# Optimization experiments

Measured on AMD Instinct MI355X. Metric: run time of the kernel, lower is better.

Reference implementation:

```python
import jax, jax.numpy as jnp
import numpy as np

EPS = 2e-05
N_H_RDG = 9   # lifting scale grid: h_j = 2**j, j=0..8
N_H_CROP = 3  # group-conv scale support: offsets 0,1,2 (dyadic index shifts)


def _scaled_kernel(w, h):
    """Resample base kernel w [O, I, K] (taps on integers centered at 0) at
    coordinates x/h via linear interpolation -> [O, I, (K-1)*h+1], with the
    R+ Haar-measure normalization 1/h (psi_h(x) = psi(x/h)/h)."""
    K = w.shape[-1]
    Kh = (K - 1) * h + 1
    m = jnp.arange(K, dtype=jnp.float32) - K // 2
    x = (jnp.arange(Kh, dtype=jnp.float32) - Kh // 2) / h
    hat = jnp.maximum(0.0, 1.0 - jnp.abs(x[:, None] - m[None, :]))  # [Kh, K]
    return jnp.einsum('oim,xm->oix', w, hat) / h


def _conv1d_same(x, k):
    pad = (k.shape[-1] - 1) // 2
    return jax.lax.conv_general_dilated(
        x, k, window_strides=(1,), padding=[(pad, pad)],
        dimension_numbers=('NCH', 'OIH', 'NCH'))


def _pool_r1(x, stride):
    # max pool over the spatial (last) axis only: kernel 4, pad 1 each side
    return jax.lax.reduce_window(
        x, -jnp.inf, jax.lax.max,
        window_dimensions=(1, 1, 1, 4), window_strides=(1, 1, 1, stride),
        padding=((0, 0), (0, 0), (0, 0), (1, 1)))


def _bn(x, g, b):
    # BatchNorm2d over [B, C, H_scale, L], training-mode batch stats
    mu = jnp.mean(x, axis=(0, 2, 3), keepdims=True)
    var = jnp.var(x, axis=(0, 2, 3), keepdims=True)
    return (x - mu) * jax.lax.rsqrt(var + EPS) * g[None, :, None, None] + b[None, :, None, None]


def _forward(x, w1, w2, w3, g1, b1, g2, b2, g3, b3, fw1, fb1, fw2, fb2, fw3, fb3):
    B = x.shape[0]
    # --- c1: GConvRdG lifting, scales h_j = 2**j, j=0..8 ---
    out = jnp.stack([_conv1d_same(x, _scaled_kernel(w1, 2 ** j))
                     for j in range(N_H_RDG)], axis=2)      # [B,16,9,16]
    out = _bn(jax.nn.relu(_pool_r1(out, 2)), g1, b1)        # [B,16,9,8]
    # --- c2: GConvGG, h_crop=True: out scale j uses in scales j..j+2 ---
    O2, I2 = w2.shape[0], w2.shape[1]
    w2r = w2.reshape(O2, I2 * N_H_CROP, 3)
    H2 = out.shape[2] - (N_H_CROP - 1)  # 7
    out = jnp.stack([
        _conv1d_same(out[:, :, j:j + N_H_CROP, :].reshape(B, I2 * N_H_CROP, -1),
                     _scaled_kernel(w2r, 2 ** j))
        for j in range(H2)], axis=2)                        # [B,32,7,8]
    out = _bn(jax.nn.relu(_pool_r1(out, 2)), g2, b2)        # [B,32,7,4]
    # --- c3: GConvGG with 1x1 spatial kernel ---
    w3s = w3[:, :, :, 0]  # [64,32,3]
    H3 = out.shape[2] - (N_H_CROP - 1)  # 5
    out = jnp.stack([
        jnp.einsum('oik,bikl->bol', w3s, out[:, :, j:j + N_H_CROP, :]) / (2.0 ** j)
        for j in range(H3)], axis=2)                        # [B,64,5,4]
    out = _bn(jax.nn.relu(_pool_r1(out, 4)), g3, b3)        # [B,64,5,1]
    # --- MLP head (dropout is identity in eval) ---
    out = out.reshape(B, -1)                                # [B,320]
    out = out @ fw1.T + fb1
    out = out @ fw2.T + fb2
    return out @ fw3.T + fb3                                # [B,17]


def setup_inputs() -> dict:
    key = jax.random.key(0)
    ks = jax.random.split(key, 7)
    B = 4096
    x = jax.random.normal(ks[0], (B, 6, 16), dtype=jnp.float32)
    w1 = jax.random.normal(ks[1], (16, 6, 7), dtype=jnp.float32) * (6 * 7) ** -0.5
    w2 = jax.random.normal(ks[2], (32, 16, 3, 3), dtype=jnp.float32) * (16 * 3 * 3) ** -0.5
    w3 = jax.random.normal(ks[3], (64, 32, 3, 1), dtype=jnp.float32) * (32 * 3) ** -0.5
    fw1 = jax.random.normal(ks[4], (16, 320), dtype=jnp.float32) * 320 ** -0.5
    fw2 = jax.random.normal(ks[5], (16, 16), dtype=jnp.float32) * 16 ** -0.5
    fw3 = jax.random.normal(ks[6], (17, 16), dtype=jnp.float32) * 16 ** -0.5
    return {
        'x': x, 'w1': w1, 'w2': w2, 'w3': w3,
        'g1': jnp.ones(16), 'b1': jnp.zeros(16),
        'g2': jnp.ones(32), 'b2': jnp.zeros(32),
        'g3': jnp.ones(64), 'b3': jnp.zeros(64),
        'fw1': fw1, 'fb1': jnp.zeros(16),
        'fw2': fw2, 'fb2': jnp.zeros(16),
        'fw3': fw3, 'fb3': jnp.zeros(17),
    }


def reference(x, w1, w2, w3, g1, b1, g2, b2, g3, b3, fw1, fb1, fw2, fb2, fw3, fb3):
    return _forward(x, w1, w2, w3, g1, b1, g2, b2, g3, b3, fw1, fb1, fw2, fb2, fw3, fb3)
```

## Files before the change

kernel.cpp:

```cpp
#include <hip/hip_runtime.h>

#define EPS 2e-5f

using short8  = __attribute__((ext_vector_type(8))) short;
using floatx4 = __attribute__((ext_vector_type(4))) float;

static __device__ inline unsigned short f2bf(float f) {
    unsigned u = __float_as_uint(f);
    u += 0x7fffu + ((u >> 16) & 1u);
    return (unsigned short)(u >> 16);
}
static __device__ inline float bf2f(short s) {
    return __uint_as_float(((unsigned)(unsigned short)s) << 16);
}
static __device__ inline short8 scale8(short8 v, float sc) {
    short8 r;
    #pragma unroll
    for (int e = 0; e < 8; ++e) r[e] = (short)f2bf(bf2f(v[e]) * sc);
    return r;
}


__global__ void __launch_bounds__(256) kSa(const float* __restrict__ w1,
                                           unsigned short* __restrict__ W1f,
                                           float* __restrict__ stats) {
    int gid = blockIdx.x * 256 + threadIdx.x;
    if (gid < 256) stats[gid] = 0.f;
    int j  = gid / 24576;
    int r  = gid % 24576;
    int T  = r / 1536;
    int r2 = r % 1536;
    int ks = r2 / 512;
    int r3 = r2 % 512;
    int ln = r3 >> 3, e = r3 & 7;
    int n  = T * 16 + (ln & 15);
    int kk = ks * 32 + (ln >> 4) * 8 + e;
    int o = n >> 4, t = n & 15;
    int i = kk >> 4, s = kk & 15;
    int h = 1 << j;
    int d = s - t;
    float val = 0.f;
    if (d >= -3 * h && d <= 3 * h) {
        float df = (float)d / (float)h;
        #pragma unroll
        for (int m = 0; m < 7; ++m) {
            float hat = fmaxf(0.f, 1.f - fabsf(df - (float)(m - 3)));
            val += w1[(o * 6 + i) * 7 + m] * hat;
        }
        val /= (float)h;
    }
    W1f[gid] = f2bf(val);
}

__global__ void __launch_bounds__(256) k1(const float* __restrict__ x,
                                          const unsigned short* __restrict__ W1f,
                                          const float* __restrict__ w2,
                                          unsigned short* __restrict__ p1,
                                          unsigned short* __restrict__ W2r,
                                          float* __restrict__ S,
                                          float* __restrict__ stats1, int B) {
    __shared__ float z[32 * 276];
    __shared__ float lsS[256], lsQ[256];
    int tid = threadIdx.x;

    if (blockIdx.y == 9) {
        int base = blockIdx.x * 256 + tid;
        for (int g = base; g < 688128; g += 32768) {
            int fs = g >> 9;
            int ln = (g >> 3) & 63, e = g & 7;
            int j  = fs / 192;
            int rm = fs % 192;
            int T  = rm / 12, ks = rm % 12;
            int col = T * 16 + (ln & 15);
            int k   = ks * 32 + (ln >> 4) * 8 + e;
            int o = col >> 3, t = col & 7;
            int ic = k >> 3, s = k & 7;
            int i = ic / 3, c = ic % 3;
            int h = 1 << j;
            int d = s - t;
            float raw = 0.f;
            if (d >= -h && d <= h) {
                float df = (float)d / (float)h;
                #pragma unroll
                for (int m = 0; m < 3; ++m) {
                    float hat = fmaxf(0.f, 1.f - fabsf(df - (float)(m - 1)));
                    raw += w2[((o * 16 + i) * 3 + c) * 3 + m] * hat;
                }
                raw /= (float)h;
            }
            W2r[g] = f2bf(raw);
        }
        for (int g = base; g < 28672; g += 32768) {
            int j = g >> 12;
            int r = g & 4095;
            int i = r >> 8;
            int col = r & 255;
            int o = col >> 3, t = col & 7;
            int h = 1 << j;
            float acc = 0.f;
            #pragma unroll
            for (int c = 0; c < 3; ++c) {
                const float* wr = &w2[((o * 16 + i) * 3 + c) * 3];
                #pragma unroll
                for (int s = 0; s < 8; ++s) {
                    int d = s - t;
                    if (d >= -h && d <= h) {
                        float df = (float)d / (float)h;
                        float raw = 0.f;
                        #pragma unroll
                        for (int m = 0; m < 3; ++m) {
                            float hat = fmaxf(0.f, 1.f - fabsf(df - (float)(m - 1)));
                            raw += wr[m] * hat;
                        }
                        acc += raw / (float)h;
                    }
                }
            }
            S[g] = acc;
        }
        return;
    }

    int j = blockIdx.y;
    int wav = tid >> 6, lane = tid & 63;
    int quad = lane >> 4, l15 = lane & 15;
    int msub = wav & 1, nh = wav >> 1;
    int b0 = blockIdx.x * 32;
    floatx4 acc[8];
    #pragma unroll
    for (int T = 0; T < 8; ++T) acc[T] = floatx4{0.f, 0.f, 0.f, 0.f};
    const float* xr = x + (size_t)(b0 + msub * 16 + l15) * 96;
    const short8* Bj = (const short8*)W1f + (size_t)(j * 16) * 3 * 64;
    #pragma unroll
    for (int ks = 0; ks < 3; ++ks) {
        int k0 = ks * 32 + quad * 8;
        floatx4 v0 = *(const floatx4*)(xr + k0);
        floatx4 v1 = *(const floatx4*)(xr + k0 + 4);
        short8 a;
        #pragma unroll
        for (int e = 0; e < 4; ++e) {
            a[e]     = (short)f2bf(v0[e]);
            a[e + 4] = (short)f2bf(v1[e]);
        }
        #pragma unroll
        for (int T = 0; T < 8; ++T) {
            short8 b = Bj[((nh * 8 + T) * 3 + ks) * 64 + lane];
            acc[T] = __builtin_amdgcn_mfma_f32_16x16x32_bf16(a, b, acc[T], 0, 0, 0);
        }
    }
    #pragma unroll
    for (int T = 0; T < 8; ++T) {
        int col = (nh * 8 + T) * 16 + l15;
        int rb  = msub * 16 + quad * 4;
        #pragma unroll
        for (int r = 0; r < 4; ++r) z[(rb + r) * 276 + col] = acc[T][r];
    }
    __syncthreads();
    float psum = 0.f, pss = 0.f;
    #pragma unroll
    for (int i = 0; i < 2; ++i) {
        int u = tid + 256 * i;
        int row = u >> 4, o = u & 15;
        const float* zr = &z[row * 276 + o * 16];
        floatx4 q0 = ((const floatx4*)zr)[0];
        floatx4 q1 = ((const floatx4*)zr)[1];
        floatx4 q2 = ((const floatx4*)zr)[2];
        floatx4 q3 = ((const floatx4*)zr)[3];
        float t[16] = {q0[0], q0[1], q0[2], q0[3], q1[0], q1[1], q1[2], q1[3],
                       q2[0], q2[1], q2[2], q2[3], q3[0], q3[1], q3[2], q3[3]};
        short8 pk;
        #pragma unroll
        for (int tp = 0; tp < 8; ++tp) {
            int lo = (tp == 0) ? 0 : 2 * tp - 1;
            int hi = (tp == 7) ? 15 : 2 * tp + 2;
            float m = t[lo];
            for (int tt = lo + 1; tt <= hi; ++tt) m = fmaxf(m, t[tt]);
            m = fmaxf(m, 0.f);
            pk[tp] = (short)f2bf(m);
            psum += m; pss += m * m;
        }
        *(short8*)(p1 + ((size_t)j * B + b0 + row) * 128 + o * 8) = pk;
    }
    lsS[(tid & 15) * 16 + (tid >> 4)] = psum;
    lsQ[(tid & 15) * 16 + (tid >> 4)] = pss;
    __syncthreads();
    if (tid < 32) {
        int o = tid & 15;
        const float* src = (tid < 16) ? lsS : lsQ;
        float s = 0.f;
        #pragma unroll
        for (int g = 0; g < 16; ++g) s += src[o * 16 + g];
        atomicAdd(&stats1[(tid < 16 ? 0 : 16) + o], s);
    }
}

__global__ void __launch_bounds__(256) k2(const unsigned short* __restrict__ p1,
                                          const unsigned short* __restrict__ W2r,
                                          const float* __restrict__ S,
                                          const float* __restrict__ g1,
                                          const float* __restrict__ b1,
                                          const float* __restrict__ stats1,
                                          unsigned short* __restrict__ p2s,
                                          float* __restrict__ stats2,
                                          float invN1, int B) {
    __shared__ float z[32 * 260];
    __shared__ float lsS[512], lsQ[512];
    __shared__ float a1s[16], d1s[16], bias2L[256];
    int tid = threadIdx.x, j = blockIdx.y;
    int wav = tid >> 6, lane = tid & 63;
    int quad = lane >> 4, l15 = lane & 15;
    int nh = wav & 1, mp = wav >> 1;
    int b0 = blockIdx.x * 64, m0 = b0 + mp * 32;
    if (tid < 16) {
        float mu  = stats1[tid] * invN1;
        float var = stats1[16 + tid] * invN1 - mu * mu;
        float rs  = rsqrtf(var + EPS);
        a1s[tid] = g1[tid] * rs;
        d1s[tid] = b1[tid] - mu * a1s[tid];
    }
    __syncthreads();
    {
        float s = 0.f;
        const float* Sj = S + (size_t)j * 4096;
        #pragma unroll
        for (int i = 0; i < 16; ++i) s = fmaf(d1s[i], Sj[i * 256 + tid], s);
        bias2L[tid] = s;
    }
    __syncthreads();
    float biasv[8];
    #pragma unroll
    for (int T = 0; T < 8; ++T) biasv[T] = bias2L[(nh * 8 + T) * 16 + l15];
    floatx4 acc[2][8];
    #pragma unroll
    for (int mi = 0; mi < 2; ++mi)
        #pragma unroll
        for (int T = 0; T < 8; ++T) acc[mi][T] = floatx4{0.f, 0.f, 0.f, 0.f};
    const short8* Bj = (const short8*)W2r + (size_t)(j * 16) * 12 * 64;
    #pragma unroll
    for (int ks = 0; ks < 12; ++ks) {
        int icq = ks * 4 + quad;
        int i = icq / 3, c = icq - i * 3;
        float a1v = a1s[i];
        const unsigned short* ap = p1 + ((size_t)(j + c) * B + m0 + l15) * 128 + i * 8;
        short8 a0 = scale8(*(const short8*)ap, a1v);
        short8 a1 = scale8(*(const short8*)(ap + 2048), a1v);
        #pragma unroll
        for (int T = 0; T < 8; ++T) {
            short8 b = Bj[((nh * 8 + T) * 12 + ks) * 64 + lane];
            acc[0][T] = __builtin_amdgcn_mfma_f32_16x16x32_bf16(a0, b, acc[0][T], 0, 0, 0);
            acc[1][T] = __builtin_amdgcn_mfma_f32_16x16x32_bf16(a1, b, acc[1][T], 0, 0, 0);
        }
    }
    float psum[2] = {0.f, 0.f}, pss[2] = {0.f, 0.f};
    for (int pass = 0; pass < 2; ++pass) {
        __syncthreads();
        if (mp == pass) {
            #pragma unroll
            for (int T = 0; T < 8; ++T) {
                int col = (nh * 8 + T) * 16 + l15;
                #pragma unroll
                for (int mi = 0; mi < 2; ++mi) {
                    int rb = mi * 16 + quad * 4;
                    #pragma unroll
                    for (int r = 0; r < 4; ++r)
                        z[(rb + r) * 260 + col] = acc[mi][T][r] + biasv[T];
                }
            }
        }
        __syncthreads();
        #pragma unroll
        for (int i2 = 0; i2 < 2; ++i2) {
            int u = tid + 256 * i2;
            int opr = u & 15, row = u >> 4;
            const float* zr = &z[row * 260 + opr * 16];
            floatx4 q0 = ((const floatx4*)zr)[0];
            floatx4 q1 = ((const floatx4*)zr)[1];
            floatx4 q2 = ((const floatx4*)zr)[2];
            floatx4 q3 = ((const floatx4*)zr)[3];
            float ta[8] = {q0[0], q0[1], q0[2], q0[3], q1[0], q1[1], q1[2], q1[3]};
            float tb[8] = {q2[0], q2[1], q2[2], q2[3], q3[0], q3[1], q3[2], q3[3]};
            int rowg = pass * 32 + row;
            #pragma unroll
            for (int tp = 0; tp < 4; ++tp) {
                int lo = (tp == 0) ? 0 : 2 * tp - 1;
                int hi = (tp == 3) ? 7 : 2 * tp + 2;
                float m0v = ta[lo], m1v = tb[lo];
                for (int tt = lo + 1; tt <= hi; ++tt) {
                    m0v = fmaxf(m0v, ta[tt]); m1v = fmaxf(m1v, tb[tt]);
                }
                m0v = fmaxf(m0v, 0.f); m1v = fmaxf(m1v, 0.f);
                psum[0] += m0v; pss[0] += m0v * m0v;
                psum[1] += m1v; pss[1] += m1v * m1v;
                unsigned pk = (unsigned)f2bf(m0v) | ((unsigned)f2bf(m1v) << 16);
                *(unsigned*)(p2s + ((size_t)(j * 4 + tp) * B + b0 + rowg) * 32
                             + opr * 2) = pk;
            }
        }
    }
    {
        int o0 = 2 * (tid & 15), g = tid >> 4;
        lsS[o0 * 16 + g] = psum[0]; lsS[(o0 + 1) * 16 + g] = psum[1];
        lsQ[o0 * 16 + g] = pss[0];  lsQ[(o0 + 1) * 16 + g] = pss[1];
    }
    __syncthreads();
    if (tid < 64) {
        int o = tid & 31;
        const float* src = (tid < 32) ? lsS : lsQ;
        float s = 0.f;
        #pragma unroll
        for (int g = 0; g < 16; ++g) s += src[o * 16 + g];
        atomicAdd(&stats2[(tid < 32 ? 0 : 32) + o], s);
    }
}

__global__ void __launch_bounds__(256) k3(const unsigned short* __restrict__ p2s,
                                          const float* __restrict__ w3,
                                          const float* __restrict__ g2,
                                          const float* __restrict__ b2,
                                          const float* __restrict__ stats2,
                                          unsigned short* __restrict__ act3,
                                          float* __restrict__ stats3,
                                          float invN2, int B) {
    __shared__ float w3s[6144];
    __shared__ float a2s[32], d2s[32];
    __shared__ unsigned short atile[32][72];
    __shared__ float lsS[1024], lsQ[1024];
    int tid = threadIdx.x, j = blockIdx.y, b0 = blockIdx.x * 32;
    int og = tid >> 6, lane = tid & 63;
    int quad = lane >> 4, l15 = lane & 15;
    #pragma unroll
    for (int u = 0; u < 6; ++u) {
        int idx = tid * 4 + u * 1024;
        *(floatx4*)&w3s[idx] = *(const floatx4*)&w3[idx];
    }
    if (tid < 32) {
        float mu  = stats2[tid] * invN2;
        float var = stats2[32 + tid] * invN2 - mu * mu;
        float rs  = rsqrtf(var + EPS);
        a2s[tid] = g2[tid] * rs;
        d2s[tid] = b2[tid] - mu * a2s[tid];
    }
    __syncthreads();
    int o = og * 16 + l15;
    float biasacc = 0.f;
    short8 af[3];
    #pragma unroll
    for (int kf = 0; kf < 3; ++kf) {
        short8 v;
        #pragma unroll
        for (int e = 0; e < 8; ++e) {
            int i = quad * 8 + e;
            float raw = w3s[o * 96 + i * 3 + kf];
            v[e] = (short)f2bf(raw * a2s[i]);
            biasacc = fmaf(raw, d2s[i], biasacc);
        }
        af[kf] = v;
    }
    biasacc += __shfl_xor(biasacc, 16, 64);
    biasacc += __shfl_xor(biasacc, 32, 64);
    float brow[4];
    #pragma unroll
    for (int r = 0; r < 4; ++r) brow[r] = __shfl(biasacc, quad * 4 + r, 64);
    float inv = 1.f / (float)(1 << j);
    float psum[4] = {0.f, 0.f, 0.f, 0.f}, pss[4] = {0.f, 0.f, 0.f, 0.f};
    #pragma unroll
    for (int bt = 0; bt < 2; ++bt) {
        int bb = b0 + bt * 16;
        floatx4 aL0 = {0.f, 0.f, 0.f, 0.f};
        floatx4 aL1 = {0.f, 0.f, 0.f, 0.f};
        floatx4 aL2 = {0.f, 0.f, 0.f, 0.f};
        #pragma unroll
        for (int c = 0; c < 3; ++c) {
            const unsigned short* base =
                p2s + ((size_t)((j + c) * 4) * B + bb + l15) * 32 + quad * 8;
            short8 f0 = *(const short8*)base;
            short8 f1 = *(const short8*)(base + (size_t)B * 32);
            short8 f2v = *(const short8*)(base + (size_t)2 * B * 32);
            aL0 = __builtin_amdgcn_mfma_f32_16x16x32_bf16(af[c], f0, aL0, 0, 0, 0);
            aL1 = __builtin_amdgcn_mfma_f32_16x16x32_bf16(af[c], f1, aL1, 0, 0, 0);
            aL2 = __builtin_amdgcn_mfma_f32_16x16x32_bf16(af[c], f2v, aL2, 0, 0, 0);
        }
        #pragma unroll
        for (int r = 0; r < 4; ++r) {
            float vm = fmaxf(fmaxf(aL0[r], aL1[r]), aL2[r]);
            float v  = fmaxf((vm + brow[r]) * inv, 0.f);
            atile[bt * 16 + l15][og * 16 + quad * 4 + r] = f2bf(v);
            psum[r] += v; pss[r] += v * v;
        }
    }
    #pragma unroll
    for (int r = 0; r < 4; ++r) {
        lsS[(og * 16 + quad * 4 + r) * 16 + l15] = psum[r];
        lsQ[(og * 16 + quad * 4 + r) * 16 + l15] = pss[r];
    }
    __syncthreads();
    {
        int row = tid >> 3, oct = tid & 7;
        *(short8*)(act3 + ((size_t)j * B + b0 + row) * 64 + oct * 8) =
            *(const short8*)&atile[row][oct * 8];
    }
    if (tid < 128) {
        int oo = tid & 63;
        const float* src = (tid < 64) ? lsS : lsQ;
        float s = 0.f;
        #pragma unroll
        for (int g = 0; g < 16; ++g) s += src[oo * 16 + g];
        atomicAdd(&stats3[(tid < 64 ? 0 : 64) + oo], s);
    }
}

__global__ void __launch_bounds__(128) k4(const unsigned short* __restrict__ act3,
                                          const float* __restrict__ g3,
                                          const float* __restrict__ b3,
                                          const float* __restrict__ stats3,
                                          const float* __restrict__ fw1,
                                          const float* __restrict__ fb1,
                                          const float* __restrict__ fw2,
                                          const float* __restrict__ fb2,
                                          const float* __restrict__ fw3,
                                          const float* __restrict__ fb3,
                                          float* __restrict__ out,
                                          float invN3, int B) {
    __shared__ float fw1L[5120];
    __shared__ float a3s[64], d3s[64];
    __shared__ unsigned short W1s[5120];
    __shared__ float fw2s[256], fw3s[272], fb2s[16], fb3s[17], fb1f[16], tmp[4][16];
    __shared__ float hbuf[2][16][17];
    int tid = threadIdx.x;
    int wav = tid >> 6, lane = tid & 63;
    int quad = lane >> 4, l15 = lane & 15;
    #pragma unroll
    for (int u = 0; u < 10; ++u) {
        int idx = (tid + u * 128) * 4;
        *(floatx4*)&fw1L[idx] = *(const floatx4*)&fw1[idx];
    }
    if (tid < 64) {
        float mu  = stats3[tid] * invN3;
        float var = stats3[64 + tid] * invN3 - mu * mu;
        float rs  = rsqrtf(var + EPS);
        a3s[tid] = g3[tid] * rs;
        d3s[tid] = b3[tid] - mu * a3s[tid];
    }
    if (tid < 16) fb2s[tid] = fb2[tid];
    if (tid < 17) fb3s[tid] = fb3[tid];
    #pragma unroll
    for (int u = 0; u < 2; ++u) fw2s[tid + u * 128] = fw2[tid + u * 128];
    for (int idx = tid; idx < 272; idx += 128) fw3s[idx] = fw3[idx];
    __syncthreads();
    #pragma unroll
    for (int u = 0; u < 40; ++u) {
        int idx = tid + u * 128;
        int e  = idx & 7;
        int ln = (idx >> 3) & 63;
        int fs = idx >> 9;
        int jj = fs >> 1, ks = fs & 1;
        int n = ln & 15;
        int oo = ks * 32 + (ln >> 4) * 8 + e;
        W1s[idx] = f2bf(fw1L[n * 320 + oo * 5 + jj] * a3s[oo]);
    }
    if (tid < 64) {
        int f = tid & 15, ch = tid >> 4;
        float s = 0.f;
        for (int u = 0; u < 80; ++u) {
            int n = ch * 80 + u;
            s = fmaf(fw1L[f * 320 + n], d3s[n / 5], s);
        }
        tmp[ch][f] = s;
    }
    __syncthreads();
    if (tid < 16) fb1f[tid] = fb1[tid] + tmp[0][tid] + tmp[1][tid] + tmp[2][tid] + tmp[3][tid];
    __syncthreads();
    int mt = blockIdx.x * 2 + wav;
    floatx4 acc = {0.f, 0.f, 0.f, 0.f};
    #pragma unroll
    for (int jj = 0; jj < 5; ++jj)
        #pragma unroll
        for (int ks = 0; ks < 2; ++ks) {
            short8 a = *(const short8*)(act3 +
                ((size_t)jj * B + mt * 16 + l15) * 64 + ks * 32 + quad * 8);
            short8 b = *(const short8*)&W1s[((jj * 2 + ks) * 64 + lane) * 8];
            acc = __builtin_amdgcn_mfma_f32_16x16x32_bf16(a, b, acc, 0, 0, 0);
        }
    #pragma unroll
    for (int r = 0; r < 4; ++r) hbuf[wav][quad * 4 + r][l15] = acc[r] + fb1f[l15];
    __syncthreads();
    if (lane < 16) {
        int row = l15;
        float hv[16];
        #pragma unroll
        for (int n = 0; n < 16; ++n) hv[n] = hbuf[wav][row][n];
        float h2[16];
        #pragma unroll
        for (int f2 = 0; f2 < 16; ++f2) {
            float s = fb2s[f2];
            #pragma unroll
            for (int n = 0; n < 16; ++n) s = fmaf(fw2s[f2 * 16 + n], hv[n], s);
            h2[f2] = s;
        }
        float* orow = out + (size_t)(mt * 16 + row) * 17;
        #pragma unroll
        for (int f3 = 0; f3 < 17; ++f3) {
            float s = fb3s[f3];
            #pragma unroll
            for (int n = 0; n < 16; ++n) s = fmaf(fw3s[f3 * 16 + n], h2[n], s);
            orow[f3] = s;
        }
    }
}

extern "C" void kernel_launch(void* const* d_in, const int* in_sizes, int n_in,
                              void* d_out, int out_size, void* d_ws, size_t ws_size,
                              hipStream_t stream) {
    (void)n_in; (void)out_size; (void)ws_size;
    const float* x   = (const float*)d_in[0];
    const float* w1  = (const float*)d_in[1];
    const float* w2  = (const float*)d_in[2];
    const float* w3  = (const float*)d_in[3];
    const float* g1  = (const float*)d_in[4];
    const float* b1  = (const float*)d_in[5];
    const float* g2  = (const float*)d_in[6];
    const float* b2  = (const float*)d_in[7];
    const float* g3  = (const float*)d_in[8];
    const float* b3  = (const float*)d_in[9];
    const float* fw1 = (const float*)d_in[10];
    const float* fb1 = (const float*)d_in[11];
    const float* fw2 = (const float*)d_in[12];
    const float* fb2 = (const float*)d_in[13];
    const float* fw3 = (const float*)d_in[14];
    const float* fb3 = (const float*)d_in[15];
    float* out = (float*)d_out;

    int B = in_sizes[0] / 96;

    char* wsb = (char*)d_ws;
    float*          stats = (float*)wsb;
    unsigned short* W1f   = (unsigned short*)(wsb + 1024);
    unsigned short* W2r   = W1f + 221184;
    float*          S     = (float*)(W2r + 688128);
    unsigned short* p1    = (unsigned short*)(S + 28672);
    unsigned short* p2s   = p1 + (size_t)9 * B * 128;
    unsigned short* act3  = p2s + (size_t)28 * B * 32;

    float* stats1 = stats;
    float* stats2 = stats + 32;
    float* stats3 = stats + 96;

    float invN1 = 1.f / (float)(B * 72);
    float invN2 = 1.f / (float)(B * 28);
    float invN3 = 1.f / (float)(B * 5);

    kSa<<<864, 256, 0, stream>>>(w1, W1f, stats);
    k1<<<dim3(B / 32, 10), 256, 0, stream>>>(x, W1f, w2, p1, W2r, S, stats1, B);
    k2<<<dim3(B / 64, 7), 256, 0, stream>>>(p1, W2r, S, g1, b1, stats1, p2s, stats2,
                                            invN1, B);
    k3<<<dim3(B / 32, 5), 256, 0, stream>>>(p2s, w3, g2, b2, stats2, act3, stats3,
                                            invN2, B);
    k4<<<B / 32, 128, 0, stream>>>(act3, g3, b3, stats3, fw1, fb1, fw2, fb2, fw3, fb3,
                                   out, invN3, B);
}
```

Measured before the change: 174.4 us.

## Pre-permute w3/fw1 into MFMA fragment order and shrink k2/k3/k4 per-block work

```diff
diff --git a/kernel.cpp b/kernel.cpp
--- a/kernel.cpp
+++ b/kernel.cpp
@@ -55,9 +55,13 @@
 __global__ void __launch_bounds__(256) k1(const float* __restrict__ x,
                                           const unsigned short* __restrict__ W1f,
                                           const float* __restrict__ w2,
+                                          const float* __restrict__ w3,
+                                          const float* __restrict__ fw1,
                                           unsigned short* __restrict__ p1,
                                           unsigned short* __restrict__ W2r,
                                           float* __restrict__ S,
+                                          float* __restrict__ W3fF,
+                                          float* __restrict__ W1rF,
                                           float* __restrict__ stats1, int B) {
     __shared__ float z[32 * 276];
     __shared__ float lsS[256], lsQ[256];
@@ -118,6 +122,20 @@
             }
             S[g] = acc;
         }
+        for (int g = base; g < 6144; g += 32768) {
+            int e = g & 7, ln = (g >> 3) & 63, fo = g >> 9;
+            int kf = fo >> 2, og = fo & 3;
+            int o = og * 16 + (ln & 15);
+            int i = (ln >> 4) * 8 + e;
+            W3fF[g] = w3[(o * 32 + i) * 3 + kf];
+        }
+        for (int g = base; g < 5120; g += 32768) {
+            int e = g & 7, ln = (g >> 3) & 63, fo = g >> 9;
+            int jj = fo >> 1, ks = fo & 1;
+            int n = ln & 15;
+            int oo = ks * 32 + (ln >> 4) * 8 + e;
+            W1rF[g] = fw1[n * 320 + oo * 5 + jj];
+        }
         return;
     }
 
@@ -203,10 +221,11 @@
                                           unsigned short* __restrict__ p2s,
                                           float* __restrict__ stats2,
                                           float invN1, int B) {
-    __shared__ float z[32 * 260];
+    __shared__ float z[32 * 132];
     __shared__ float lsS[512], lsQ[512];
     __shared__ float a1s[16], d1s[16], bias2L[256];
-    int tid = threadIdx.x, j = blockIdx.y;
+    int tid = threadIdx.x;
+    int j = blockIdx.y >> 1, ch = blockIdx.y & 1;
     int wav = tid >> 6, lane = tid & 63;
     int quad = lane >> 4, l15 = lane & 15;
     int nh = wav & 1, mp = wav >> 1;
@@ -227,14 +246,15 @@
         bias2L[tid] = s;
     }
     __syncthreads();
-    float biasv[8];
-    #pragma unroll
-    for (int T = 0; T < 8; ++T) biasv[T] = bias2L[(nh * 8 + T) * 16 + l15];
-    floatx4 acc[2][8];
+    float biasv[4];
+    #pragma unroll
+    for (int T = 0; T < 4; ++T)
+        biasv[T] = bias2L[(ch * 8 + nh * 4 + T) * 16 + l15];
+    floatx4 acc[2][4];
     #pragma unroll
     for (int mi = 0; mi < 2; ++mi)
         #pragma unroll
-        for (int T = 0; T < 8; ++T) acc[mi][T] = floatx4{0.f, 0.f, 0.f, 0.f};
+        for (int T = 0; T < 4; ++T) acc[mi][T] = floatx4{0.f, 0.f, 0.f, 0.f};
     const short8* Bj = (const short8*)W2r + (size_t)(j * 16) * 12 * 64;
     #pragma unroll
     for (int ks = 0; ks < 12; ++ks) {
@@ -245,8 +265,8 @@
         short8 a0 = scale8(*(const short8*)ap, a1v);
         short8 a1 = scale8(*(const short8*)(ap + 2048), a1v);
         #pragma unroll
-        for (int T = 0; T < 8; ++T) {
-            short8 b = Bj[((nh * 8 + T) * 12 + ks) * 64 + lane];
+        for (int T = 0; T < 4; ++T) {
+            short8 b = Bj[((ch * 8 + nh * 4 + T) * 12 + ks) * 64 + lane];
             acc[0][T] = __builtin_amdgcn_mfma_f32_16x16x32_bf16(a0, b, acc[0][T], 0, 0, 0);
             acc[1][T] = __builtin_amdgcn_mfma_f32_16x16x32_bf16(a1, b, acc[1][T], 0, 0, 0);
         }
@@ -256,23 +276,21 @@
         __syncthreads();
         if (mp == pass) {
             #pragma unroll
-            for (int T = 0; T < 8; ++T) {
-                int col = (nh * 8 + T) * 16 + l15;
+            for (int T = 0; T < 4; ++T) {
+                int colloc = (nh * 4 + T) * 16 + l15;
                 #pragma unroll
                 for (int mi = 0; mi < 2; ++mi) {
                     int rb = mi * 16 + quad * 4;
                     #pragma unroll
                     for (int r = 0; r < 4; ++r)
-                        z[(rb + r) * 260 + col] = acc[mi][T][r] + biasv[T];
+                        z[(rb + r) * 132 + colloc] = acc[mi][T][r] + biasv[T];
                 }
             }
         }
         __syncthreads();
-        #pragma unroll
-        for (int i2 = 0; i2 < 2; ++i2) {
-            int u = tid + 256 * i2;
-            int opr = u & 15, row = u >> 4;
-            const float* zr = &z[row * 260 + opr * 16];
+        {
+            int opr = tid & 7, row = tid >> 3;
+            const float* zr = &z[row * 132 + opr * 16];
             floatx4 q0 = ((const floatx4*)zr)[0];
             floatx4 q1 = ((const floatx4*)zr)[1];
             floatx4 q2 = ((const floatx4*)zr)[2];
@@ -293,66 +311,75 @@
                 psum[1] += m1v; pss[1] += m1v * m1v;
                 unsigned pk = (unsigned)f2bf(m0v) | ((unsigned)f2bf(m1v) << 16);
                 *(unsigned*)(p2s + ((size_t)(j * 4 + tp) * B + b0 + rowg) * 32
-                             + opr * 2) = pk;
+                             + ch * 16 + opr * 2) = pk;
             }
         }
     }
     {
-        int o0 = 2 * (tid & 15), g = tid >> 4;
-        lsS[o0 * 16 + g] = psum[0]; lsS[(o0 + 1) * 16 + g] = psum[1];
-        lsQ[o0 * 16 + g] = pss[0];  lsQ[(o0 + 1) * 16 + g] = pss[1];
-    }
-    __syncthreads();
-    if (tid < 64) {
-        int o = tid & 31;
-        const float* src = (tid < 32) ? lsS : lsQ;
+        int opr = tid & 7, row = tid >> 3;
+        lsS[(opr * 2 + 0) * 32 + row] = psum[0];
+        lsS[(opr * 2 + 1) * 32 + row] = psum[1];
+        lsQ[(opr * 2 + 0) * 32 + row] = pss[0];
+        lsQ[(opr * 2 + 1) * 32 + row] = pss[1];
+    }
+    __syncthreads();
+    if (tid < 32) {
+        int oloc = tid & 15;
+        const float* src = (tid < 16) ? lsS : lsQ;
         float s = 0.f;
         #pragma unroll
-        for (int g = 0; g < 16; ++g) s += src[o * 16 + g];
-        atomicAdd(&stats2[(tid < 32 ? 0 : 32) + o], s);
+        for (int r = 0; r < 32; ++r) s += src[oloc * 32 + r];
+        atomicAdd(&stats2[(tid < 16 ? 0 : 32) + ch * 16 + oloc], s);
     }
 }
 
 __global__ void __launch_bounds__(256) k3(const unsigned short* __restrict__ p2s,
-                                          const float* __restrict__ w3,
+                                          const float* __restrict__ W3fF,
                                           const float* __restrict__ g2,
                                           const float* __restrict__ b2,
                                           const float* __restrict__ stats2,
                                           unsigned short* __restrict__ act3,
                                           float* __restrict__ stats3,
                                           float invN2, int B) {
-    __shared__ float w3s[6144];
-    __shared__ float a2s[32], d2s[32];
-    __shared__ unsigned short atile[32][72];
+    __shared__ unsigned short atile[16][72];
     __shared__ float lsS[1024], lsQ[1024];
-    int tid = threadIdx.x, j = blockIdx.y, b0 = blockIdx.x * 32;
+    int tid = threadIdx.x, j = blockIdx.y, b0 = blockIdx.x * 16;
     int og = tid >> 6, lane = tid & 63;
     int quad = lane >> 4, l15 = lane & 15;
-    #pragma unroll
-    for (int u = 0; u < 6; ++u) {
-        int idx = tid * 4 + u * 1024;
-        *(floatx4*)&w3s[idx] = *(const floatx4*)&w3[idx];
-    }
-    if (tid < 32) {
-        float mu  = stats2[tid] * invN2;
-        float var = stats2[32 + tid] * invN2 - mu * mu;
-        float rs  = rsqrtf(var + EPS);
-        a2s[tid] = g2[tid] * rs;
-        d2s[tid] = b2[tid] - mu * a2s[tid];
-    }
-    __syncthreads();
-    int o = og * 16 + l15;
+    int i0 = quad * 8;
+    floatx4 sm0 = *(const floatx4*)&stats2[i0];
+    floatx4 sm1 = *(const floatx4*)&stats2[i0 + 4];
+    floatx4 sq0 = *(const floatx4*)&stats2[32 + i0];
+    floatx4 sq1 = *(const floatx4*)&stats2[32 + i0 + 4];
+    floatx4 gg0 = *(const floatx4*)&g2[i0];
+    floatx4 gg1 = *(const floatx4*)&g2[i0 + 4];
+    floatx4 bv0 = *(const floatx4*)&b2[i0];
+    floatx4 bv1 = *(const floatx4*)&b2[i0 + 4];
+    float a2v[8], d2v[8];
+    #pragma unroll
+    for (int e = 0; e < 4; ++e) {
+        float mu = sm0[e] * invN2;
+        float var = sq0[e] * invN2 - mu * mu;
+        float rs = rsqrtf(var + EPS);
+        a2v[e] = gg0[e] * rs; d2v[e] = bv0[e] - mu * a2v[e];
+        mu = sm1[e] * invN2;
+        var = sq1[e] * invN2 - mu * mu;
+        rs = rsqrtf(var + EPS);
+        a2v[e + 4] = gg1[e] * rs; d2v[e + 4] = bv1[e] - mu * a2v[e + 4];
+    }
     float biasacc = 0.f;
     short8 af[3];
     #pragma unroll
     for (int kf = 0; kf < 3; ++kf) {
+        const float* wp = &W3fF[((size_t)(kf * 4 + og) * 64 + lane) * 8];
+        floatx4 w0 = ((const floatx4*)wp)[0];
+        floatx4 w1 = ((const floatx4*)wp)[1];
+        float wr[8] = {w0[0], w0[1], w0[2], w0[3], w1[0], w1[1], w1[2], w1[3]};
         short8 v;
         #pragma unroll
         for (int e = 0; e < 8; ++e) {
-            int i = quad * 8 + e;
-            float raw = w3s[o * 96 + i * 3 + kf];
-            v[e] = (short)f2bf(raw * a2s[i]);
-            biasacc = fmaf(raw, d2s[i], biasacc);
+            v[e] = (short)f2bf(wr[e] * a2v[e]);
+            biasacc = fmaf(wr[e], d2v[e], biasacc);
         }
         af[kf] = v;
     }
@@ -363,30 +390,26 @@
     for (int r = 0; r < 4; ++r) brow[r] = __shfl(biasacc, quad * 4 + r, 64);
     float inv = 1.f / (float)(1 << j);
     float psum[4] = {0.f, 0.f, 0.f, 0.f}, pss[4] = {0.f, 0.f, 0.f, 0.f};
-    #pragma unroll
-    for (int bt = 0; bt < 2; ++bt) {
-        int bb = b0 + bt * 16;
-        floatx4 aL0 = {0.f, 0.f, 0.f, 0.f};
-        floatx4 aL1 = {0.f, 0.f, 0.f, 0.f};
-        floatx4 aL2 = {0.f, 0.f, 0.f, 0.f};
-        #pragma unroll
-        for (int c = 0; c < 3; ++c) {
-            const unsigned short* base =
-                p2s + ((size_t)((j + c) * 4) * B + bb + l15) * 32 + quad * 8;
-            short8 f0 = *(const short8*)base;
-            short8 f1 = *(const short8*)(base + (size_t)B * 32);
-            short8 f2v = *(const short8*)(base + (size_t)2 * B * 32);
-            aL0 = __builtin_amdgcn_mfma_f32_16x16x32_bf16(af[c], f0, aL0, 0, 0, 0);
-            aL1 = __builtin_amdgcn_mfma_f32_16x16x32_bf16(af[c], f1, aL1, 0, 0, 0);
-            aL2 = __builtin_amdgcn_mfma_f32_16x16x32_bf16(af[c], f2v, aL2, 0, 0, 0);
-        }
-        #pragma unroll
-        for (int r = 0; r < 4; ++r) {
-            float vm = fmaxf(fmaxf(aL0[r], aL1[r]), aL2[r]);
-            float v  = fmaxf((vm + brow[r]) * inv, 0.f);
-            atile[bt * 16 + l15][og * 16 + quad * 4 + r] = f2bf(v);
-            psum[r] += v; pss[r] += v * v;
-        }
+    floatx4 aL0 = {0.f, 0.f, 0.f, 0.f};
+    floatx4 aL1 = {0.f, 0.f, 0.f, 0.f};
+    floatx4 aL2 = {0.f, 0.f, 0.f, 0.f};
+    #pragma unroll
+    for (int c = 0; c < 3; ++c) {
+        const unsigned short* base =
+            p2s + ((size_t)((j + c) * 4) * B + b0 + l15) * 32 + quad * 8;
+        short8 f0 = *(const short8*)base;
+        short8 f1 = *(const short8*)(base + (size_t)B * 32);
+        short8 f2v = *(const short8*)(base + (size_t)2 * B * 32);
+        aL0 = __builtin_amdgcn_mfma_f32_16x16x32_bf16(af[c], f0, aL0, 0, 0, 0);
+        aL1 = __builtin_amdgcn_mfma_f32_16x16x32_bf16(af[c], f1, aL1, 0, 0, 0);
+        aL2 = __builtin_amdgcn_mfma_f32_16x16x32_bf16(af[c], f2v, aL2, 0, 0, 0);
+    }
+    #pragma unroll
+    for (int r = 0; r < 4; ++r) {
+        float vm = fmaxf(fmaxf(aL0[r], aL1[r]), aL2[r]);
+        float v  = fmaxf((vm + brow[r]) * inv, 0.f);
+        atile[l15][og * 16 + quad * 4 + r] = f2bf(v);
+        psum[r] += v; pss[r] += v * v;
     }
     #pragma unroll
     for (int r = 0; r < 4; ++r) {
@@ -394,7 +417,7 @@
         lsQ[(og * 16 + quad * 4 + r) * 16 + l15] = pss[r];
     }
     __syncthreads();
-    {
+    if (tid < 128) {
         int row = tid >> 3, oct = tid & 7;
         *(short8*)(act3 + ((size_t)j * B + b0 + row) * 64 + oct * 8) =
             *(const short8*)&atile[row][oct * 8];
@@ -409,68 +432,53 @@
     }
 }
 
-__global__ void __launch_bounds__(128) k4(const unsigned short* __restrict__ act3,
-                                          const float* __restrict__ g3,
-                                          const float* __restrict__ b3,
-                                          const float* __restrict__ stats3,
-                                          const float* __restrict__ fw1,
-                                          const float* __restrict__ fb1,
-                                          const float* __restrict__ fw2,
-                                          const float* __restrict__ fb2,
-                                          const float* __restrict__ fw3,
-                                          const float* __restrict__ fb3,
-                                          float* __restrict__ out,
-                                          float invN3, int B) {
-    __shared__ float fw1L[5120];
-    __shared__ float a3s[64], d3s[64];
-    __shared__ unsigned short W1s[5120];
-    __shared__ float fw2s[256], fw3s[272], fb2s[16], fb3s[17], fb1f[16], tmp[4][16];
-    __shared__ float hbuf[2][16][17];
+__global__ void __launch_bounds__(64) k4(const unsigned short* __restrict__ act3,
+                                         const float* __restrict__ W1rF,
+                                         const float* __restrict__ g3,
+                                         const float* __restrict__ b3,
+                                         const float* __restrict__ stats3,
+                                         const float* __restrict__ fw1,
+                                         const float* __restrict__ fb1,
+                                         const float* __restrict__ fw2,
+                                         const float* __restrict__ fb2,
+                                         const float* __restrict__ fw3,
+                                         const float* __restrict__ fb3,
+                                         float* __restrict__ out,
+                                         float invN3, int B) {
+    __shared__ float a3s[64], d3s[64], fb1f[16], tmp[4][16];
+    __shared__ float fw2s[256], fw3s[272], fb2s[16], fb3s[17];
+    __shared__ float hbuf[16][17];
     int tid = threadIdx.x;
-    int wav = tid >> 6, lane = tid & 63;
-    int quad = lane >> 4, l15 = lane & 15;
-    #pragma unroll
-    for (int u = 0; u < 10; ++u) {
-        int idx = (tid + u * 128) * 4;
-        *(floatx4*)&fw1L[idx] = *(const floatx4*)&fw1[idx];
-    }
-    if (tid < 64) {
+    int quad = tid >> 4, l15 = tid & 15;
+    {
         float mu  = stats3[tid] * invN3;
         float var = stats3[64 + tid] * invN3 - mu * mu;
         float rs  = rsqrtf(var + EPS);
-        a3s[tid] = g3[tid] * rs;
-        d3s[tid] = b3[tid] - mu * a3s[tid];
-    }
+        float a   = g3[tid] * rs;
+        a3s[tid] = a;
+        d3s[tid] = b3[tid] - mu * a;
+    }
+    #pragma unroll
+    for (int u = 0; u < 4; ++u) fw2s[tid + u * 64] = fw2[tid + u * 64];
+    for (int idx = tid; idx < 272; idx += 64) fw3s[idx] = fw3[idx];
     if (tid < 16) fb2s[tid] = fb2[tid];
     if (tid < 17) fb3s[tid] = fb3[tid];
-    #pragma unroll
-    for (int u = 0; u < 2; ++u) fw2s[tid + u * 128] = fw2[tid + u * 128];
-    for (int idx = tid; idx < 272; idx += 128) fw3s[idx] = fw3[idx];
-    __syncthreads();
-    #pragma unroll
-    for (int u = 0; u < 40; ++u) {
-        int idx = tid + u * 128;
-        int e  = idx & 7;
-        int ln = (idx >> 3) & 63;
-        int fs = idx >> 9;
-        int jj = fs >> 1, ks = fs & 1;
-        int n = ln & 15;
-        int oo = ks * 32 + (ln >> 4) * 8 + e;
-        W1s[idx] = f2bf(fw1L[n * 320 + oo * 5 + jj] * a3s[oo]);
-    }
-    if (tid < 64) {
+    __syncthreads();
+    {
         int f = tid & 15, ch = tid >> 4;
         float s = 0.f;
         for (int u = 0; u < 80; ++u) {
             int n = ch * 80 + u;
-            s = fmaf(fw1L[f * 320 + n], d3s[n / 5], s);
+            s = fmaf(fw1[f * 320 + n], d3s[n / 5], s);
         }
         tmp[ch][f] = s;
     }
-    __syncthreads();
-    if (tid < 16) fb1f[tid] = fb1[tid] + tmp[0][tid] + tmp[1][tid] + tmp[2][tid] + tmp[3][tid];
-    __syncthreads();
-    int mt = blockIdx.x * 2 + wav;
+    float a3v[2][8];
+    #pragma unroll
+    for (int ks = 0; ks < 2; ++ks)
+        #pragma unroll
+        for (int e = 0; e < 8; ++e) a3v[ks][e] = a3s[ks * 32 + quad * 8 + e];
+    int mt = blockIdx.x;
     floatx4 acc = {0.f, 0.f, 0.f, 0.f};
     #pragma unroll
     for (int jj = 0; jj < 5; ++jj)
@@ -478,17 +486,29 @@
         for (int ks = 0; ks < 2; ++ks) {
             short8 a = *(const short8*)(act3 +
                 ((size_t)jj * B + mt * 16 + l15) * 64 + ks * 32 + quad * 8);
-            short8 b = *(const short8*)&W1s[((jj * 2 + ks) * 64 + lane) * 8];
+            const float* wp = &W1rF[((size_t)(jj * 2 + ks) * 64 + tid) * 8];
+            floatx4 w0 = ((const floatx4*)wp)[0];
+            floatx4 w1 = ((const floatx4*)wp)[1];
+            short8 b;
+            #pragma unroll
+            for (int e = 0; e < 4; ++e) {
+                b[e]     = (short)f2bf(w0[e] * a3v[ks][e]);
+                b[e + 4] = (short)f2bf(w1[e] * a3v[ks][e + 4]);
+            }
             acc = __builtin_amdgcn_mfma_f32_16x16x32_bf16(a, b, acc, 0, 0, 0);
         }
-    #pragma unroll
-    for (int r = 0; r < 4; ++r) hbuf[wav][quad * 4 + r][l15] = acc[r] + fb1f[l15];
-    __syncthreads();
-    if (lane < 16) {
+    __syncthreads();
+    if (tid < 16) fb1f[tid] = fb1[tid] + tmp[0][tid] + tmp[1][tid]
+                            + tmp[2][tid] + tmp[3][tid];
+    __syncthreads();
+    #pragma unroll
+    for (int r = 0; r < 4; ++r) hbuf[quad * 4 + r][l15] = acc[r] + fb1f[l15];
+    __syncthreads();
+    if (tid < 16) {
         int row = l15;
         float hv[16];
         #pragma unroll
-        for (int n = 0; n < 16; ++n) hv[n] = hbuf[wav][row][n];
+        for (int n = 0; n < 16; ++n) hv[n] = hbuf[row][n];
         float h2[16];
         #pragma unroll
         for (int f2 = 0; f2 < 16; ++f2) {
@@ -537,7 +557,9 @@
     unsigned short* W1f   = (unsigned short*)(wsb + 1024);
     unsigned short* W2r   = W1f + 221184;
     float*          S     = (float*)(W2r + 688128);
-    unsigned short* p1    = (unsigned short*)(S + 28672);
+    float*          W3fF  = S + 28672;
+    float*          W1rF  = W3fF + 6144;
+    unsigned short* p1    = (unsigned short*)(W1rF + 5120);
     unsigned short* p2s   = p1 + (size_t)9 * B * 128;
     unsigned short* act3  = p2s + (size_t)28 * B * 32;
 
@@ -550,11 +572,12 @@
     float invN3 = 1.f / (float)(B * 5);
 
     kSa<<<864, 256, 0, stream>>>(w1, W1f, stats);
-    k1<<<dim3(B / 32, 10), 256, 0, stream>>>(x, W1f, w2, p1, W2r, S, stats1, B);
-    k2<<<dim3(B / 64, 7), 256, 0, stream>>>(p1, W2r, S, g1, b1, stats1, p2s, stats2,
-                                            invN1, B);
-    k3<<<dim3(B / 32, 5), 256, 0, stream>>>(p2s, w3, g2, b2, stats2, act3, stats3,
+    k1<<<dim3(B / 32, 10), 256, 0, stream>>>(x, W1f, w2, w3, fw1, p1, W2r, S,
+                                             W3fF, W1rF, stats1, B);
+    k2<<<dim3(B / 64, 14), 256, 0, stream>>>(p1, W2r, S, g1, b1, stats1, p2s, stats2,
+                                             invN1, B);
+    k3<<<dim3(B / 16, 5), 256, 0, stream>>>(p2s, W3fF, g2, b2, stats2, act3, stats3,
                                             invN2, B);
-    k4<<<B / 32, 128, 0, stream>>>(act3, g3, b3, stats3, fw1, fb1, fw2, fb2, fw3, fb3,
-                                   out, invN3, B);
-}
+    k4<<<B / 16, 64, 0, stream>>>(act3, W1rF, g3, b3, stats3, fw1, fb1, fw2, fb2,
+                                  fw3, fb3, out, invN3, B);
+}
```

After: 190.2 us. 1.09x slower.
